# Kernel optimization log

Hardware: AMD Instinct MI355X
Metric: run time of the kernel (lower is better)

The kernel has to match this reference:

```python
import jax, jax.numpy as jnp
import numpy as np

FEATURE_DIM = 128
EDGE_DIM = 32
N_NODES = 10000
BATCH = 4
N_EDGES = 640000
TEMPERATURE = 0.66
POWER_ITERS = 5


def spectral_normalize(W):
    # torch.nn.utils.spectral_norm: divide W by largest singular value estimated
    # via power iteration; u, v are treated as constants (no grad).
    # W: [out, in]
    u = jnp.ones((W.shape[0],), W.dtype) / jnp.sqrt(jnp.asarray(W.shape[0], W.dtype))
    for _ in range(POWER_ITERS):
        v = W.T @ u
        v = v / (jnp.linalg.norm(v) + 1e-12)
        u = W @ v
        u = u / (jnp.linalg.norm(u) + 1e-12)
    u = jax.lax.stop_gradient(u)
    v = jax.lax.stop_gradient(v)
    sigma = u @ (W @ v)
    return W / sigma


def setup_inputs() -> dict:
    key = jax.random.key(0)
    ks = jax.random.split(key, 8)
    node_feat = jax.random.normal(ks[0], (BATCH, N_NODES, FEATURE_DIM), dtype=jnp.float32)
    batch_ids = jax.random.randint(ks[1], (N_EDGES,), 0, BATCH)
    src_nodes = jax.random.randint(ks[2], (N_EDGES,), 0, N_NODES)
    tgt_nodes = jax.random.randint(ks[3], (N_EDGES,), 0, N_NODES)
    in_dim = 2 * FEATURE_DIM + 1  # src_feat ++ tgt_feat ++ distance
    # kaiming_normal_(nonlinearity='relu'): std = sqrt(2 / fan_in)
    W1 = jax.random.normal(ks[4], (EDGE_DIM, in_dim), jnp.float32) * np.sqrt(2.0 / in_dim)
    b1 = jnp.zeros((EDGE_DIM,), jnp.float32)
    W2 = jax.random.normal(ks[5], (EDGE_DIM, EDGE_DIM), jnp.float32) * np.sqrt(2.0 / EDGE_DIM)
    b2 = jnp.zeros((EDGE_DIM,), jnp.float32)
    bound = 0.1 * np.sqrt(6.0 / (EDGE_DIM + 1))
    W3 = jax.random.uniform(ks[6], (1, EDGE_DIM), jnp.float32, -bound, bound)
    b3 = jnp.ones((1,), jnp.float32)
    return {"node_feat": node_feat, "W1": W1, "b1": b1, "W2": W2, "b2": b2,
            "W3": W3, "b3": b3, "batch_ids": batch_ids,
            "src_nodes": src_nodes, "tgt_nodes": tgt_nodes}


def reference(node_feat, W1, b1, W2, b2, W3, b3, batch_ids, src_nodes, tgt_nodes):
    # per-edge gather of endpoint features  [E, D]
    src_feat = node_feat[batch_ids, src_nodes]
    tgt_feat = node_feat[batch_ids, tgt_nodes]
    dist = jnp.linalg.norm(src_feat - tgt_feat, axis=-1, keepdims=True)  # [E,1]
    edge_features = jnp.concatenate([src_feat, tgt_feat, dist], axis=-1)  # [E, 2D+1]
    # spectral-norm MLP (dropout is identity at eval / in this reference)
    h = jax.nn.relu(edge_features @ spectral_normalize(W1).T + b1)
    h = jax.nn.relu(h @ spectral_normalize(W2).T + b2)
    logAlpha = (h @ spectral_normalize(W3).T + b3).squeeze(-1)  # [E]
    logAlpha = jnp.clip(logAlpha, -5.0, 5.0)
    edge_weights = jax.nn.sigmoid(logAlpha / TEMPERATURE)
    return edge_weights, logAlpha
```

## Files before the change

kernel.cpp:

```cpp
#include <hip/hip_runtime.h>
#include <hip/hip_fp16.h>
#include <math.h>

#define FEATD 128
#define NNODES 10000
#define NBATCH 4
#define NROWS (NBATCH*NNODES)

#define OFF_I1   0
#define OFF_W1L  8
#define OFF_W2   64
#define OFF_W3   1088
#define OFF_W2H  1120
#define OFF_P16  4096
#define P16_FLOATS (NROWS*64/2)
#define OFF_F16  (OFF_P16 + P16_FLOATS)
#define F16_FLOATS (NROWS*FEATD/2)
#define OFF_FBWT OFF_P16

#define WSTRIDE 68

typedef _Float16 h2 __attribute__((ext_vector_type(2)));
union U32H2 { unsigned u; h2 h; };
union U4H2  { uint4 u; h2 h[4]; };

#if defined(__has_builtin)
#if __has_builtin(__builtin_amdgcn_fdot2)
#define HAVE_FDOT2 1
#endif
#endif

__device__ __forceinline__ float fdot2f(h2 a, h2 b, float c) {
#ifdef HAVE_FDOT2
  return __builtin_amdgcn_fdot2(a, b, c, false);
#else
  return c + (float)a[0] * (float)b[0] + (float)a[1] * (float)b[1];
#endif
}

template <int M, int K>
__device__ float spectral_sigma_t(const float* __restrict__ Wg,
                                  float* sW, float* u, float* v, volatile float* red) {
  int tid = threadIdx.x;
  int wid = tid >> 6, lid = tid & 63;
  int j8 = tid >> 3, l8 = tid & 7;
  for (int i = tid; i < M * K; i += 256) sW[i] = Wg[i];
  if (tid < M) u[tid] = 1.0f;
  __syncthreads();
  float invu = 1.0f / sqrtf((float)M);
  float invv = 0.f;

  for (int it = 0; it < 5; ++it) {
    float p = 0.f;
    for (int k = tid; k < K; k += 256) {
      float a = 0.f;
      #pragma unroll
      for (int j = 0; j < M; ++j) a += sW[j * K + k] * u[j];
      a *= invu;
      v[k] = a;
      p += a * a;
    }
    #pragma unroll
    for (int off = 1; off < 64; off <<= 1) p += __shfl_xor(p, off, 64);
    if (lid == 0) red[wid] = p;
    __syncthreads();
    p = red[0] + red[1] + red[2] + red[3];
    invv = 1.0f / (sqrtf(p) + 1e-12f);

    float a = 0.f;
    if (j8 < M) {
      #pragma unroll
      for (int k = l8; k < K; k += 8) a += sW[j8 * K + k] * v[k];
      a *= invv;
    }
    a += __shfl_xor(a, 1, 64);
    a += __shfl_xor(a, 2, 64);
    a += __shfl_xor(a, 4, 64);
    float q = 0.f;
    if (j8 < M && l8 == 0) { u[j8] = a; q = a * a; }
    #pragma unroll
    for (int off = 1; off < 64; off <<= 1) q += __shfl_xor(q, off, 64);
    if (lid == 0) red[4 + wid] = q;
    __syncthreads();
    q = red[4] + red[5] + red[6] + red[7];
    invu = 1.0f / (sqrtf(q) + 1e-12f);
  }

  float a = 0.f;
  if (j8 < M) {
    #pragma unroll
    for (int k = l8; k < K; k += 8) a += sW[j8 * K + k] * v[k];
  }
  a += __shfl_xor(a, 1, 64);
  a += __shfl_xor(a, 2, 64);
  a += __shfl_xor(a, 4, 64);
  float s = (j8 < M && l8 == 0) ? a * u[j8] : 0.f;
  #pragma unroll
  for (int off = 1; off < 64; off <<= 1) s += __shfl_xor(s, off, 64);
  if (lid == 0) red[wid] = s;
  __syncthreads();
  float sig = (red[0] + red[1] + red[2] + red[3]) * invu * invv;
  __syncthreads();
  return sig;
}

__global__ __launch_bounds__(256, 4) void prep_kernel(const float* __restrict__ feat,
                                                      const float* __restrict__ W1,
                                                      const float* __restrict__ W2,
                                                      const float* __restrict__ W3,
                                                      float* __restrict__ ws,
                                                      int doF16) {
  __shared__ float sA[128 * WSTRIDE];
  __shared__ float u[32], v[257];
  __shared__ float red[8];
  int tid = threadIdx.x;

  if (blockIdx.x == 0) {
    float sig1 = spectral_sigma_t<32, 257>(W1, sA, u, v, red);
    float i1 = 1.0f / sig1;
    if (tid == 0) ws[OFF_I1] = i1;
    for (int j = tid; j < 32; j += 256) ws[OFF_W1L + j] = sA[j * 257 + 256] * i1;
    __syncthreads();
    float sig2 = spectral_sigma_t<32, 32>(W2, sA, u, v, red);
    float i2 = 1.0f / sig2;
    for (int idx = tid; idx < 1024; idx += 256) ws[OFF_W2 + idx] = sA[idx] * i2;
    unsigned* w2h = (unsigned*)(ws + OFF_W2H);
    for (int idx = tid; idx < 512; idx += 256) {
      int j = idx >> 4, q = idx & 15;
      U32H2 pk;
      pk.h[0] = (_Float16)(sA[j * 32 + 2 * q] * i2);
      pk.h[1] = (_Float16)(sA[j * 32 + 2 * q + 1] * i2);
      w2h[idx] = pk.u;
    }
    __syncthreads();
    float sig3 = spectral_sigma_t<1, 32>(W3, sA, u, v, red);
    float i3 = 1.0f / sig3;
    for (int k = tid; k < 32; k += 256) ws[OFF_W3 + k] = sA[k] * i3;
    return;
  }

  for (int idx = tid; idx < 32 * 257; idx += 256) {
    int j = idx / 257, c = idx - j * 257;
    float w = W1[idx];
    if (c < 128) sA[c * WSTRIDE + j] = w;
    else if (c < 256) sA[(c - 128) * WSTRIDE + 32 + j] = w;
  }
  __syncthreads();

  __half* p16 = (__half*)(ws + OFF_P16);
  __half* f16 = (__half*)(ws + OFF_F16);
  int rg = tid >> 4;
  int jg = (tid & 15) << 2;
  int slice = tid & 15;
  int r0 = (blockIdx.x - 1) * 64 + rg * 4;
  const float4* F0 = (const float4*)&feat[(size_t)(r0 + 0) * FEATD];
  const float4* F1 = (const float4*)&feat[(size_t)(r0 + 1) * FEATD];
  const float4* F2 = (const float4*)&feat[(size_t)(r0 + 2) * FEATD];
  const float4* F3 = (const float4*)&feat[(size_t)(r0 + 3) * FEATD];
  float acc[4][4] = {{0,0,0,0},{0,0,0,0},{0,0,0,0},{0,0,0,0}};

  #pragma unroll 2
  for (int k4 = 0; k4 < 32; ++k4) {
    float4 f0 = F0[k4], f1 = F1[k4], f2 = F2[k4], f3 = F3[k4];
    if (doF16 && (k4 >> 1) == slice) {
      U32H2 a, b; uint2 pk;
      a.h[0]=(_Float16)f0.x; a.h[1]=(_Float16)f0.y; b.h[0]=(_Float16)f0.z; b.h[1]=(_Float16)f0.w;
      pk.x=a.u; pk.y=b.u; *(uint2*)((char*)f16 + (size_t)(r0+0)*256 + (size_t)k4*8) = pk;
      a.h[0]=(_Float16)f1.x; a.h[1]=(_Float16)f1.y; b.h[0]=(_Float16)f1.z; b.h[1]=(_Float16)f1.w;
      pk.x=a.u; pk.y=b.u; *(uint2*)((char*)f16 + (size_t)(r0+1)*256 + (size_t)k4*8) = pk;
      a.h[0]=(_Float16)f2.x; a.h[1]=(_Float16)f2.y; b.h[0]=(_Float16)f2.z; b.h[1]=(_Float16)f2.w;
      pk.x=a.u; pk.y=b.u; *(uint2*)((char*)f16 + (size_t)(r0+2)*256 + (size_t)k4*8) = pk;
      a.h[0]=(_Float16)f3.x; a.h[1]=(_Float16)f3.y; b.h[0]=(_Float16)f3.z; b.h[1]=(_Float16)f3.w;
      pk.x=a.u; pk.y=b.u; *(uint2*)((char*)f16 + (size_t)(r0+3)*256 + (size_t)k4*8) = pk;
    }
    #pragma unroll
    for (int kk = 0; kk < 4; ++kk) {
      int k = 4 * k4 + kk;
      float4 w = *(const float4*)&sA[k * WSTRIDE + jg];
      float e0 = (kk == 0) ? f0.x : (kk == 1) ? f0.y : (kk == 2) ? f0.z : f0.w;
      float e1 = (kk == 0) ? f1.x : (kk == 1) ? f1.y : (kk == 2) ? f1.z : f1.w;
      float e2 = (kk == 0) ? f2.x : (kk == 1) ? f2.y : (kk == 2) ? f2.z : f2.w;
      float e3 = (kk == 0) ? f3.x : (kk == 1) ? f3.y : (kk == 2) ? f3.z : f3.w;
      acc[0][0] += e0 * w.x; acc[0][1] += e0 * w.y; acc[0][2] += e0 * w.z; acc[0][3] += e0 * w.w;
      acc[1][0] += e1 * w.x; acc[1][1] += e1 * w.y; acc[1][2] += e1 * w.z; acc[1][3] += e1 * w.w;
      acc[2][0] += e2 * w.x; acc[2][1] += e2 * w.y; acc[2][2] += e2 * w.z; acc[2][3] += e2 * w.w;
      acc[3][0] += e3 * w.x; acc[3][1] += e3 * w.y; acc[3][2] += e3 * w.z; acc[3][3] += e3 * w.w;
    }
  }
  #pragma unroll
  for (int r = 0; r < 4; ++r) {
    U32H2 a, b;
    a.h[0] = (_Float16)acc[r][0]; a.h[1] = (_Float16)acc[r][1];
    b.h[0] = (_Float16)acc[r][2]; b.h[1] = (_Float16)acc[r][3];
    uint2 o; o.x = a.u; o.y = b.u;
    *(uint2*)((char*)p16 + (size_t)(r0 + r) * 128 + (size_t)jg * 2) = o;
  }
}

__device__ __forceinline__ float grp_dist_f16(uint4 au, uint4 bu) {
  U4H2 a, b; a.u = au; b.u = bu;
  float ssd = 0.f;
  #pragma unroll
  for (int p = 0; p < 4; ++p) { h2 d = a.h[p] - b.h[p]; ssd = fdot2f(d, d, ssd); }
  ssd += __shfl_xor(ssd, 1, 64);
  ssd += __shfl_xor(ssd, 2, 64);
  ssd += __shfl_xor(ssd, 4, 64);
  ssd += __shfl_xor(ssd, 8, 64);
  return sqrtf(ssd);
}

__device__ __forceinline__ unsigned h1pack(unsigned puv, unsigned quv, float dist, float i1,
                                           float w1l0, float w1l1, float bb0, float bb1) {
  U32H2 p, q; p.u = puv; q.u = quv;
  float h0  = fmaxf(fmaf((float)p.h[0] + (float)q.h[0], i1, fmaf(dist, w1l0, bb0)), 0.f);
  float h1v = fmaxf(fmaf((float)p.h[1] + (float)q.h[1], i1, fmaf(dist, w1l1, bb1)), 0.f);
  U32H2 r; r.h[0] = (_Float16)h0; r.h[1] = (_Float16)h1v;
  return r.u;
}

template <bool F16>
__global__ __launch_bounds__(256, 8) void edge_fused(const float* __restrict__ feat,
                                                     const float* __restrict__ ws,
                                                     const float* __restrict__ b1,
                                                     const float* __restrict__ b2,
                                                     const float* __restrict__ b3,
                                                     const int* __restrict__ bids,
                                                     const int* __restrict__ srcs,
                                                     const int* __restrict__ tgts,
                                                     float* __restrict__ out, int E) {
  __shared__ unsigned ht[256 * 17];
  __shared__ int sRS[256], sRT[256];
  int tid = threadIdx.x;
  int lane = tid & 15;
  int grp  = tid >> 4;

  const __half* feat16 = (const __half*)(ws + OFF_F16);
  const __half* p16    = (const __half*)(ws + OFF_P16);
  const unsigned* w2h  = (const unsigned*)(ws + OFF_W2H);

  float i1 = ws[OFF_I1];
  int j0 = 2 * lane;
  float w1l0 = ws[OFF_W1L + j0];
  float w1l1 = ws[OFF_W1L + j0 + 1];
  float bb0  = b1[j0];
  float bb1  = b1[j0 + 1];
  float bias3 = b3[0];

  for (int base = blockIdx.x * 256; base < E; base += gridDim.x * 256) {
    int e0 = base + tid;
    if (e0 < E) {
      int b = bids[e0];
      sRS[tid] = b * NNODES + srcs[e0];
      sRT[tid] = b * NNODES + tgts[e0];
    }
    __syncthreads();

    if (F16 && (base + 256 <= E)) {
      #pragma unroll 1
      for (int rr = 0; rr < 8; ++rr) {
        int el0 = (rr * 2 + 0) * 16 + grp;
        int el1 = (rr * 2 + 1) * 16 + grp;
        int rs0 = sRS[el0], rt0 = sRT[el0];
        int rs1 = sRS[el1], rt1 = sRT[el1];
        uint4 a0 = *(const uint4*)((const char*)feat16 + ((size_t)rs0 << 8) + (lane << 4));
        uint4 c0 = *(const uint4*)((const char*)feat16 + ((size_t)rt0 << 8) + (lane << 4));
        uint4 a1 = *(const uint4*)((const char*)feat16 + ((size_t)rs1 << 8) + (lane << 4));
        uint4 c1 = *(const uint4*)((const char*)feat16 + ((size_t)rt1 << 8) + (lane << 4));
        unsigned pu0 = *(const unsigned*)((const char*)p16 + ((size_t)rs0 << 7) + (lane << 2));
        unsigned qu0 = *(const unsigned*)((const char*)p16 + ((size_t)rt0 << 7) + 64 + (lane << 2));
        unsigned pu1 = *(const unsigned*)((const char*)p16 + ((size_t)rs1 << 7) + (lane << 2));
        unsigned qu1 = *(const unsigned*)((const char*)p16 + ((size_t)rt1 << 7) + 64 + (lane << 2));
        float d0 = grp_dist_f16(a0, c0);
        float d1 = grp_dist_f16(a1, c1);
        ht[el0 * 17 + lane] = h1pack(pu0, qu0, d0, i1, w1l0, w1l1, bb0, bb1);
        ht[el1 * 17 + lane] = h1pack(pu1, qu1, d1, i1, w1l0, w1l1, bb0, bb1);
      }
    } else {
      #pragma unroll 2
      for (int rr = 0; rr < 16; ++rr) {
        int el = rr * 16 + grp;
        int e  = base + el;
        if (e < E) {
          int rs = sRS[el], rt = sRT[el];
          float dist;
          if (F16) {
            uint4 au = *(const uint4*)((const char*)feat16 + ((size_t)rs << 8) + (lane << 4));
            uint4 bu = *(const uint4*)((const char*)feat16 + ((size_t)rt << 8) + (lane << 4));
            dist = grp_dist_f16(au, bu);
          } else {
            const float4* A  = (const float4*)&feat[(size_t)rs * FEATD];
            const float4* Bp = (const float4*)&feat[(size_t)rt * FEATD];
            float ssd = 0.f;
            #pragma unroll
            for (int p = 0; p < 2; ++p) {
              float4 a = A[lane * 2 + p], c = Bp[lane * 2 + p];
              float dx = a.x - c.x, dy = a.y - c.y, dz = a.z - c.z, dw = a.w - c.w;
              ssd += dx * dx + dy * dy + dz * dz + dw * dw;
            }
            ssd += __shfl_xor(ssd, 1, 64);
            ssd += __shfl_xor(ssd, 2, 64);
            ssd += __shfl_xor(ssd, 4, 64);
            ssd += __shfl_xor(ssd, 8, 64);
            dist = sqrtf(ssd);
          }
          unsigned puv = *(const unsigned*)((const char*)p16 + ((size_t)rs << 7) + (lane << 2));
          unsigned quv = *(const unsigned*)((const char*)p16 + ((size_t)rt << 7) + 64 + (lane << 2));
          ht[el * 17 + lane] = h1pack(puv, quv, dist, i1, w1l0, w1l1, bb0, bb1);
        }
      }
    }
    __syncthreads();

    int e = base + tid;
    if (e < E) {
      unsigned hrow[16];
      #pragma unroll
      for (int q = 0; q < 16; ++q) hrow[q] = ht[tid * 17 + q];
      float la = bias3;
      #pragma unroll
      for (int j = 0; j < 32; ++j) {
        float acc = b2[j];
        #pragma unroll
        for (int q = 0; q < 16; ++q) {
          U32H2 w; w.u = w2h[j * 16 + q];
          U32H2 h; h.u = hrow[q];
          acc = fdot2f(w.h, h.h, acc);
        }
        la += ws[OFF_W3 + j] * fmaxf(acc, 0.f);
      }
      la = fminf(fmaxf(la, -5.f), 5.f);
      out[e]     = 1.0f / (1.0f + exp2f(la * -2.18590179f));
      out[E + e] = la;
    }
    __syncthreads();
  }
}

__global__ __launch_bounds__(256) void spectral_full(const float* __restrict__ W1,
                                                     const float* __restrict__ W2,
                                                     const float* __restrict__ W3,
                                                     float* __restrict__ ws) {
  __shared__ float sA[32 * 257];
  __shared__ float u[32], v[257];
  __shared__ float red[8];
  int tid = threadIdx.x;
  float sig1 = spectral_sigma_t<32, 257>(W1, sA, u, v, red);
  float i1 = 1.0f / sig1;
  for (int idx = tid; idx < 128 * 64; idx += 256) {
    int k = idx >> 6, jj = idx & 63;
    float w = (jj < 32) ? sA[jj * 257 + k] : sA[(jj - 32) * 257 + 128 + k];
    ws[OFF_FBWT + idx] = w * i1;
  }
  for (int j = tid; j < 32; j += 256) ws[OFF_W1L + j] = sA[j * 257 + 256] * i1;
  __syncthreads();
  float sig2 = spectral_sigma_t<32, 32>(W2, sA, u, v, red);
  float i2 = 1.0f / sig2;
  for (int idx = tid; idx < 1024; idx += 256) ws[OFF_W2 + idx] = sA[idx] * i2;
  __syncthreads();
  float sig3 = spectral_sigma_t<1, 32>(W3, sA, u, v, red);
  float i3 = 1.0f / sig3;
  for (int k = tid; k < 32; k += 256) ws[OFF_W3 + k] = sA[k] * i3;
}

__global__ __launch_bounds__(256) void edge_kernel_nop(const float* __restrict__ feat,
                                                       const float* __restrict__ ws,
                                                       const float* __restrict__ b1,
                                                       const float* __restrict__ b2,
                                                       const float* __restrict__ b3,
                                                       const int* __restrict__ bids,
                                                       const int* __restrict__ srcs,
                                                       const int* __restrict__ tgts,
                                                       float* __restrict__ out, int E) {
  __shared__ float sWt[128 * 64];
  __shared__ float sW2[1024];
  __shared__ float sW3[32], sW1l[32], sB1[32], sB2[32];
  int tid = threadIdx.x;
  for (int i = tid * 4; i < 128 * 64; i += 256 * 4)
    *(float4*)&sWt[i] = *(const float4*)&ws[OFF_FBWT + i];
  for (int i = tid; i < 1024; i += 256) sW2[i] = ws[OFF_W2 + i];
  if (tid < 32) {
    sW3[tid]  = ws[OFF_W3 + tid];
    sW1l[tid] = ws[OFF_W1L + tid];
    sB1[tid]  = b1[tid];
    sB2[tid]  = b2[tid];
  }
  __syncthreads();
  float bias3 = b3[0];

  for (int e = blockIdx.x * 256 + tid; e < E; e += gridDim.x * 256) {
    int b = bids[e], s = srcs[e], t = tgts[e];
    const float4* A  = (const float4*)&feat[(size_t)(b * NNODES + s) * FEATD];
    const float4* Bp = (const float4*)&feat[(size_t)(b * NNODES + t) * FEATD];
    float ssd = 0.f;
    float h1p[32];
    #pragma unroll
    for (int j = 0; j < 32; ++j) h1p[j] = 0.f;
    #pragma unroll 1
    for (int k4 = 0; k4 < 32; ++k4) {
      float4 a = A[k4], c = Bp[k4];
      float dx = a.x - c.x, dy = a.y - c.y, dz = a.z - c.z, dw = a.w - c.w;
      ssd += dx * dx + dy * dy + dz * dz + dw * dw;
      #pragma unroll
      for (int kk = 0; kk < 4; ++kk) {
        int k = 4 * k4 + kk;
        float fa = (kk == 0) ? a.x : (kk == 1) ? a.y : (kk == 2) ? a.z : a.w;
        float fc = (kk == 0) ? c.x : (kk == 1) ? c.y : (kk == 2) ? c.z : c.w;
        #pragma unroll
        for (int q = 0; q < 8; ++q) {
          float4 w0 = *(const float4*)&sWt[k * 64 + 4 * q];
          float4 w1 = *(const float4*)&sWt[k * 64 + 32 + 4 * q];
          h1p[4*q+0] += fa * w0.x + fc * w1.x;
          h1p[4*q+1] += fa * w0.y + fc * w1.y;
          h1p[4*q+2] += fa * w0.z + fc * w1.z;
          h1p[4*q+3] += fa * w0.w + fc * w1.w;
        }
      }
    }
    float dist = sqrtf(ssd);
    float h1[32];
    #pragma unroll
    for (int j = 0; j < 32; ++j)
      h1[j] = fmaxf(h1p[j] + dist * sW1l[j] + sB1[j], 0.f);
    float la = bias3;
    #pragma unroll
    for (int j = 0; j < 32; ++j) {
      float acc = sB2[j];
      #pragma unroll
      for (int q = 0; q < 8; ++q) {
        float4 w = *(const float4*)&sW2[j * 32 + 4 * q];
        acc += w.x * h1[4 * q] + w.y * h1[4 * q + 1] + w.z * h1[4 * q + 2] + w.w * h1[4 * q + 3];
      }
      la += sW3[j] * fmaxf(acc, 0.f);
    }
    la = fminf(fmaxf(la, -5.f), 5.f);
    out[e]     = 1.0f / (1.0f + __expf(-la / 0.66f));
    out[E + e] = la;
  }
}

extern "C" void kernel_launch(void* const* d_in, const int* in_sizes, int n_in,
                              void* d_out, int out_size, void* d_ws, size_t ws_size,
                              hipStream_t stream) {
  const float* feat = (const float*)d_in[0];
  const float* W1   = (const float*)d_in[1];
  const float* b1   = (const float*)d_in[2];
  const float* W2   = (const float*)d_in[3];
  const float* b2   = (const float*)d_in[4];
  const float* W3   = (const float*)d_in[5];
  const float* b3   = (const float*)d_in[6];
  const int* bids   = (const int*)d_in[7];
  const int* srcs   = (const int*)d_in[8];
  const int* tgts   = (const int*)d_in[9];
  float* out = (float*)d_out;
  float* ws  = (float*)d_ws;
  int E = in_sizes[7];

  size_t need_p   = (size_t)OFF_F16 * sizeof(float);
  size_t need_f16 = (size_t)(OFF_F16 + F16_FLOATS) * sizeof(float);
  int egrid = (E + 255) / 256;

  if (ws_size >= need_f16) {
    prep_kernel<<<dim3(626), dim3(256), 0, stream>>>(feat, W1, W2, W3, ws, 1);
    edge_fused<true><<<dim3(egrid), dim3(256), 0, stream>>>(feat, ws, b1, b2, b3,
                                                            bids, srcs, tgts, out, E);
  } else if (ws_size >= need_p) {
    prep_kernel<<<dim3(626), dim3(256), 0, stream>>>(feat, W1, W2, W3, ws, 0);
    edge_fused<false><<<dim3(egrid), dim3(256), 0, stream>>>(feat, ws, b1, b2, b3,
                                                             bids, srcs, tgts, out, E);
  } else {
    spectral_full<<<dim3(1), dim3(256), 0, stream>>>(W1, W2, W3, ws);
    edge_kernel_nop<<<dim3(egrid), dim3(256), 0, stream>>>(feat, ws, b1, b2, b3,
                                                           bids, srcs, tgts, out, E);
  }
}
```

Measured before the change: 103.0 us.

## Move spectral power iteration into a single-wavefront register kernel

Power iteration for the spectral norms now runs in a separate 64-thread kernel that keeps W1 columns and W2 in registers and uses wavefront shuffles, with no shared memory or block barriers. W3's sigma is computed in closed form as its L2 norm, since it has only one row. The projection work becomes its own kernel without the special block 0, so the serial spectral block no longer sits on the critical path of a 626-block grid. The cost is an extra kernel launch that runs serially on one wavefront, and it no longer writes the fp32 W2 copy, which only matters if some consumer still reads it.

```diff
diff --git a/kernel.cpp b/kernel.cpp
--- a/kernel.cpp
+++ b/kernel.cpp
@@ -38,106 +38,128 @@
 #endif
 }
 
-template <int M, int K>
-__device__ float spectral_sigma_t(const float* __restrict__ Wg,
-                                  float* sW, float* u, float* v, volatile float* red) {
-  int tid = threadIdx.x;
-  int wid = tid >> 6, lid = tid & 63;
-  int j8 = tid >> 3, l8 = tid & 7;
-  for (int i = tid; i < M * K; i += 256) sW[i] = Wg[i];
-  if (tid < M) u[tid] = 1.0f;
-  __syncthreads();
-  float invu = 1.0f / sqrtf((float)M);
-  float invv = 0.f;
+__device__ __forceinline__ float bfly64(float x) {
+  x += __shfl_xor(x, 1, 64);
+  x += __shfl_xor(x, 2, 64);
+  x += __shfl_xor(x, 4, 64);
+  x += __shfl_xor(x, 8, 64);
+  x += __shfl_xor(x, 16, 64);
+  x += __shfl_xor(x, 32, 64);
+  return x;
+}
+
+__global__ __launch_bounds__(64, 1) void spectral64(const float* __restrict__ W1,
+                                                    const float* __restrict__ W2,
+                                                    const float* __restrict__ W3,
+                                                    float* __restrict__ ws) {
+  int lane = threadIdx.x;
+
+  float col[4][32];
+  float c256[32];
+  #pragma unroll
+  for (int m = 0; m < 4; ++m)
+    #pragma unroll
+    for (int j = 0; j < 32; ++j)
+      col[m][j] = W1[j * 257 + 64 * m + lane];
+  #pragma unroll
+  for (int j = 0; j < 32; ++j) c256[j] = W1[j * 257 + 256];
+
+  float u[32];
+  #pragma unroll
+  for (int j = 0; j < 32; ++j) u[j] = 1.0f;
+  float invu = 0.17677669529663687f;
+  float nu = 0.f;
 
   for (int it = 0; it < 5; ++it) {
-    float p = 0.f;
-    for (int k = tid; k < K; k += 256) {
-      float a = 0.f;
-      #pragma unroll
-      for (int j = 0; j < M; ++j) a += sW[j * K + k] * u[j];
-      a *= invu;
-      v[k] = a;
-      p += a * a;
-    }
-    #pragma unroll
-    for (int off = 1; off < 64; off <<= 1) p += __shfl_xor(p, off, 64);
-    if (lid == 0) red[wid] = p;
-    __syncthreads();
-    p = red[0] + red[1] + red[2] + red[3];
-    invv = 1.0f / (sqrtf(p) + 1e-12f);
-
+    float v0 = 0.f, v1 = 0.f, v2 = 0.f, v3 = 0.f, a4 = 0.f;
+    #pragma unroll
+    for (int j = 0; j < 32; ++j) {
+      v0 += col[0][j] * u[j];
+      v1 += col[1][j] * u[j];
+      v2 += col[2][j] * u[j];
+      v3 += col[3][j] * u[j];
+      a4 += c256[j] * u[j];
+    }
+    v0 *= invu; v1 *= invu; v2 *= invu; v3 *= invu;
+    float v4 = (lane == 0) ? a4 * invu : 0.f;
+    float nv = v0 * v0 + v1 * v1 + v2 * v2 + v3 * v3 + v4 * v4;
+    nv = bfly64(nv);
+    float invv = 1.0f / (sqrtf(nv) + 1e-12f);
+
+    nu = 0.f;
+    #pragma unroll
+    for (int j = 0; j < 32; ++j) {
+      float b = (col[0][j] * v0 + col[1][j] * v1 + col[2][j] * v2 +
+                 col[3][j] * v3 + c256[j] * v4) * invv;
+      b = bfly64(b);
+      u[j] = b;
+      nu += b * b;
+    }
+    invu = 1.0f / (sqrtf(nu) + 1e-12f);
+  }
+  float sig1 = nu * invu;
+  float i1 = 1.0f / sig1;
+  if (lane == 0) {
+    ws[OFF_I1] = i1;
+    #pragma unroll
+    for (int j = 0; j < 32; ++j) ws[OFF_W1L + j] = c256[j] * i1;
+  }
+
+  float wc[32];
+  #pragma unroll
+  for (int j = 0; j < 32; ++j)
+    wc[j] = (lane < 32) ? W2[j * 32 + (lane & 31)] : 0.f;
+
+  float u2[32];
+  #pragma unroll
+  for (int j = 0; j < 32; ++j) u2[j] = 1.0f;
+  float invu2 = 0.17677669529663687f;
+  float nu2 = 0.f;
+
+  for (int it = 0; it < 5; ++it) {
     float a = 0.f;
-    if (j8 < M) {
-      #pragma unroll
-      for (int k = l8; k < K; k += 8) a += sW[j8 * K + k] * v[k];
-      a *= invv;
-    }
-    a += __shfl_xor(a, 1, 64);
-    a += __shfl_xor(a, 2, 64);
-    a += __shfl_xor(a, 4, 64);
-    float q = 0.f;
-    if (j8 < M && l8 == 0) { u[j8] = a; q = a * a; }
-    #pragma unroll
-    for (int off = 1; off < 64; off <<= 1) q += __shfl_xor(q, off, 64);
-    if (lid == 0) red[4 + wid] = q;
-    __syncthreads();
-    q = red[4] + red[5] + red[6] + red[7];
-    invu = 1.0f / (sqrtf(q) + 1e-12f);
-  }
-
-  float a = 0.f;
-  if (j8 < M) {
-    #pragma unroll
-    for (int k = l8; k < K; k += 8) a += sW[j8 * K + k] * v[k];
-  }
-  a += __shfl_xor(a, 1, 64);
-  a += __shfl_xor(a, 2, 64);
-  a += __shfl_xor(a, 4, 64);
-  float s = (j8 < M && l8 == 0) ? a * u[j8] : 0.f;
-  #pragma unroll
-  for (int off = 1; off < 64; off <<= 1) s += __shfl_xor(s, off, 64);
-  if (lid == 0) red[wid] = s;
-  __syncthreads();
-  float sig = (red[0] + red[1] + red[2] + red[3]) * invu * invv;
-  __syncthreads();
-  return sig;
-}
-
-__global__ __launch_bounds__(256, 4) void prep_kernel(const float* __restrict__ feat,
+    #pragma unroll
+    for (int j = 0; j < 32; ++j) a += wc[j] * u2[j];
+    a *= invu2;
+    float nv = bfly64(a * a);
+    float invv = 1.0f / (sqrtf(nv) + 1e-12f);
+    nu2 = 0.f;
+    #pragma unroll
+    for (int j = 0; j < 32; ++j) {
+      float b = wc[j] * a * invv;
+      b = bfly64(b);
+      u2[j] = b;
+      nu2 += b * b;
+    }
+    invu2 = 1.0f / (sqrtf(nu2) + 1e-12f);
+  }
+  float sig2 = nu2 * invu2;
+  float i2 = 1.0f / sig2;
+
+  unsigned* w2h = (unsigned*)(ws + OFF_W2H);
+  #pragma unroll
+  for (int j = 0; j < 32; ++j) {
+    float val = wc[j] * i2;
+    float oth = __shfl_xor(val, 1, 64);
+    if (lane < 32 && (lane & 1) == 0) {
+      U32H2 pk;
+      pk.h[0] = (_Float16)val;
+      pk.h[1] = (_Float16)oth;
+      w2h[j * 16 + (lane >> 1)] = pk.u;
+    }
+  }
+
+  float w3v = (lane < 32) ? W3[lane & 31] : 0.f;
+  float s3 = bfly64(w3v * w3v);
+  if (lane < 32) ws[OFF_W3 + lane] = w3v / (sqrtf(s3) + 1e-12f);
+}
+
+__global__ __launch_bounds__(256, 4) void proj_kernel(const float* __restrict__ feat,
                                                       const float* __restrict__ W1,
-                                                      const float* __restrict__ W2,
-                                                      const float* __restrict__ W3,
                                                       float* __restrict__ ws,
                                                       int doF16) {
   __shared__ float sA[128 * WSTRIDE];
-  __shared__ float u[32], v[257];
-  __shared__ float red[8];
   int tid = threadIdx.x;
-
-  if (blockIdx.x == 0) {
-    float sig1 = spectral_sigma_t<32, 257>(W1, sA, u, v, red);
-    float i1 = 1.0f / sig1;
-    if (tid == 0) ws[OFF_I1] = i1;
-    for (int j = tid; j < 32; j += 256) ws[OFF_W1L + j] = sA[j * 257 + 256] * i1;
-    __syncthreads();
-    float sig2 = spectral_sigma_t<32, 32>(W2, sA, u, v, red);
-    float i2 = 1.0f / sig2;
-    for (int idx = tid; idx < 1024; idx += 256) ws[OFF_W2 + idx] = sA[idx] * i2;
-    unsigned* w2h = (unsigned*)(ws + OFF_W2H);
-    for (int idx = tid; idx < 512; idx += 256) {
-      int j = idx >> 4, q = idx & 15;
-      U32H2 pk;
-      pk.h[0] = (_Float16)(sA[j * 32 + 2 * q] * i2);
-      pk.h[1] = (_Float16)(sA[j * 32 + 2 * q + 1] * i2);
-      w2h[idx] = pk.u;
-    }
-    __syncthreads();
-    float sig3 = spectral_sigma_t<1, 32>(W3, sA, u, v, red);
-    float i3 = 1.0f / sig3;
-    for (int k = tid; k < 32; k += 256) ws[OFF_W3 + k] = sA[k] * i3;
-    return;
-  }
 
   for (int idx = tid; idx < 32 * 257; idx += 256) {
     int j = idx / 257, c = idx - j * 257;
@@ -152,7 +174,7 @@
   int rg = tid >> 4;
   int jg = (tid & 15) << 2;
   int slice = tid & 15;
-  int r0 = (blockIdx.x - 1) * 64 + rg * 4;
+  int r0 = blockIdx.x * 64 + rg * 4;
   const float4* F0 = (const float4*)&feat[(size_t)(r0 + 0) * FEATD];
   const float4* F1 = (const float4*)&feat[(size_t)(r0 + 1) * FEATD];
   const float4* F2 = (const float4*)&feat[(size_t)(r0 + 2) * FEATD];
@@ -336,6 +358,69 @@
   }
 }
 
+template <int M, int K>
+__device__ float spectral_sigma_t(const float* __restrict__ Wg,
+                                  float* sW, float* u, float* v, volatile float* red) {
+  int tid = threadIdx.x;
+  int wid = tid >> 6, lid = tid & 63;
+  int j8 = tid >> 3, l8 = tid & 7;
+  for (int i = tid; i < M * K; i += 256) sW[i] = Wg[i];
+  if (tid < M) u[tid] = 1.0f;
+  __syncthreads();
+  float invu = 1.0f / sqrtf((float)M);
+  float invv = 0.f;
+  for (int it = 0; it < 5; ++it) {
+    float p = 0.f;
+    for (int k = tid; k < K; k += 256) {
+      float a = 0.f;
+      #pragma unroll
+      for (int j = 0; j < M; ++j) a += sW[j * K + k] * u[j];
+      a *= invu;
+      v[k] = a;
+      p += a * a;
+    }
+    #pragma unroll
+    for (int off = 1; off < 64; off <<= 1) p += __shfl_xor(p, off, 64);
+    if (lid == 0) red[wid] = p;
+    __syncthreads();
+    p = red[0] + red[1] + red[2] + red[3];
+    invv = 1.0f / (sqrtf(p) + 1e-12f);
+    float a = 0.f;
+    if (j8 < M) {
+      #pragma unroll
+      for (int k = l8; k < K; k += 8) a += sW[j8 * K + k] * v[k];
+      a *= invv;
+    }
+    a += __shfl_xor(a, 1, 64);
+    a += __shfl_xor(a, 2, 64);
+    a += __shfl_xor(a, 4, 64);
+    float q = 0.f;
+    if (j8 < M && l8 == 0) { u[j8] = a; q = a * a; }
+    #pragma unroll
+    for (int off = 1; off < 64; off <<= 1) q += __shfl_xor(q, off, 64);
+    if (lid == 0) red[4 + wid] = q;
+    __syncthreads();
+    q = red[4] + red[5] + red[6] + red[7];
+    invu = 1.0f / (sqrtf(q) + 1e-12f);
+  }
+  float a = 0.f;
+  if (j8 < M) {
+    #pragma unroll
+    for (int k = l8; k < K; k += 8) a += sW[j8 * K + k] * v[k];
+  }
+  a += __shfl_xor(a, 1, 64);
+  a += __shfl_xor(a, 2, 64);
+  a += __shfl_xor(a, 4, 64);
+  float s = (j8 < M && l8 == 0) ? a * u[j8] : 0.f;
+  #pragma unroll
+  for (int off = 1; off < 64; off <<= 1) s += __shfl_xor(s, off, 64);
+  if (lid == 0) red[wid] = s;
+  __syncthreads();
+  float sig = (red[0] + red[1] + red[2] + red[3]) * invu * invv;
+  __syncthreads();
+  return sig;
+}
+
 __global__ __launch_bounds__(256) void spectral_full(const float* __restrict__ W1,
                                                      const float* __restrict__ W2,
                                                      const float* __restrict__ W3,
@@ -460,11 +545,13 @@
   int egrid = (E + 255) / 256;
 
   if (ws_size >= need_f16) {
-    prep_kernel<<<dim3(626), dim3(256), 0, stream>>>(feat, W1, W2, W3, ws, 1);
+    spectral64<<<dim3(1), dim3(64), 0, stream>>>(W1, W2, W3, ws);
+    proj_kernel<<<dim3(625), dim3(256), 0, stream>>>(feat, W1, ws, 1);
     edge_fused<true><<<dim3(egrid), dim3(256), 0, stream>>>(feat, ws, b1, b2, b3,
                                                             bids, srcs, tgts, out, E);
   } else if (ws_size >= need_p) {
-    prep_kernel<<<dim3(626), dim3(256), 0, stream>>>(feat, W1, W2, W3, ws, 0);
+    spectral64<<<dim3(1), dim3(64), 0, stream>>>(W1, W2, W3, ws);
+    proj_kernel<<<dim3(625), dim3(256), 0, stream>>>(feat, W1, ws, 0);
     edge_fused<false><<<dim3(egrid), dim3(256), 0, stream>>>(feat, ws, b1, b2, b3,
                                                              bids, srcs, tgts, out, E);
   } else {
```

Result: slower. 120.8 us (+17.3%).
